# Optimization experiments

Measured on AMD Instinct MI355X. Metric: run time of the kernel, lower is better.

Reference implementation:

```python
import jax, jax.numpy as jnp
import numpy as np

B, S, D = 2, 2048, 2048
HQ, HK, HD = 16, 8, 128          # query heads, kv heads, head_dim
EPS = 1e-6
ROPE_THETA = 10000.0
SCALE = HD ** -0.5


def setup_inputs() -> dict:
    key = jax.random.key(0)
    ks = jax.random.split(key, 6)
    s = lambda fan_in: 1.0 / np.sqrt(fan_in)
    return {
        "hidden_states": jax.random.normal(ks[0], (B, S, D), jnp.float32),
        "positions": jnp.arange(S, dtype=jnp.int32),
        "Wq": jax.random.normal(ks[1], (D, HQ * HD), jnp.float32) * s(D),
        "Wk": jax.random.normal(ks[2], (D, HK * HD), jnp.float32) * s(D),
        "Wv": jax.random.normal(ks[3], (D, HK * HD), jnp.float32) * s(D),
        "Wo": jax.random.normal(ks[4], (HQ * HD, D), jnp.float32) * s(HQ * HD),
        "q_norm_w": jnp.ones((HD,), jnp.float32),
        "k_norm_w": jnp.ones((HD,), jnp.float32),
    }


def _rmsnorm(x, w):
    # RMSNorm over last (head_dim) axis, as in q_norm/k_norm
    var = jnp.mean(jnp.square(x), axis=-1, keepdims=True)
    return x * jax.lax.rsqrt(var + EPS) * w


def _rope(x, positions):
    # x: [B, S, H, HD]; rotate_half-style RoPE (Qwen3 convention)
    half = HD // 2
    inv_freq = 1.0 / (ROPE_THETA ** (jnp.arange(0, half, dtype=jnp.float32) / half))
    angles = positions.astype(jnp.float32)[:, None] * inv_freq[None, :]  # [S, half]
    cos = jnp.cos(angles)[None, :, None, :]  # [1, S, 1, half]
    sin = jnp.sin(angles)[None, :, None, :]
    x1, x2 = x[..., :half], x[..., half:]
    return jnp.concatenate([x1 * cos - x2 * sin, x2 * cos + x1 * sin], axis=-1)


def reference(hidden_states, positions, Wq, Wk, Wv, Wo, q_norm_w, k_norm_w):
    b, s, _ = hidden_states.shape
    q = (hidden_states @ Wq).reshape(b, s, HQ, HD)
    k = (hidden_states @ Wk).reshape(b, s, HK, HD)
    v = (hidden_states @ Wv).reshape(b, s, HK, HD)

    q = _rmsnorm(q, q_norm_w)
    k = _rmsnorm(k, k_norm_w)

    q = _rope(q, positions)
    k = _rope(k, positions)

    # GQA: repeat KV heads to match query heads
    groups = HQ // HK
    k = jnp.repeat(k, groups, axis=2)  # [B, S, HQ, HD]
    v = jnp.repeat(v, groups, axis=2)

    scores = jnp.einsum("bqhd,bkhd->bhqk", q, k) * SCALE  # [B, HQ, S, S]
    causal = jnp.tril(jnp.ones((s, s), dtype=bool))
    scores = jnp.where(causal[None, None], scores, jnp.float32(-jnp.inf))
    attn = jax.nn.softmax(scores, axis=-1)

    out = jnp.einsum("bhqk,bkhd->bqhd", attn, v).reshape(b, s, HQ * HD)
    return out @ Wo
```

## Files before the change

kernel.cpp:

```cpp
#include <hip/hip_runtime.h>
#include <cstdint>
#include <cstddef>

typedef _Float16 half8 __attribute__((ext_vector_type(8)));
typedef _Float16 half4 __attribute__((ext_vector_type(4)));
typedef float f32x4 __attribute__((ext_vector_type(4)));

#define DI __device__ __forceinline__

DI void gld_lds16(void* sp, const void* gp) {
  __builtin_amdgcn_global_load_lds(
      (const __attribute__((address_space(1))) void*)gp,
      (__attribute__((address_space(3))) void*)sp, 16, 0, 0);
}

__global__ __launch_bounds__(256) void prep(const float* __restrict__ hs,
                                            const float* __restrict__ Wq,
                                            const float* __restrict__ Wk,
                                            const float* __restrict__ Wv,
                                            const float* __restrict__ Wo,
                                            _Float16* __restrict__ Xh,
                                            _Float16* __restrict__ Wqkvt,
                                            _Float16* __restrict__ Wot) {
  const int bid = blockIdx.x;
  if (bid >= 12288) {
    const int i = (bid - 12288) * 256 + threadIdx.x;
    const float4* p = (const float4*)hs + (size_t)i * 2;
    const float4 a = p[0], b = p[1];
    half8 h;
    h[0] = (_Float16)a.x; h[1] = (_Float16)a.y; h[2] = (_Float16)a.z; h[3] = (_Float16)a.w;
    h[4] = (_Float16)b.x; h[5] = (_Float16)b.y; h[6] = (_Float16)b.z; h[7] = (_Float16)b.w;
    *(half8*)(Xh + (size_t)i * 8) = h;
    return;
  }
  const float* in;
  _Float16* outp;
  int C, t;
  if (bid < 4096)      { in = Wq; outp = Wqkvt;                        C = 2048; t = bid; }
  else if (bid < 6144) { in = Wk; outp = Wqkvt + (size_t)2048 * 2048;  C = 1024; t = bid - 4096; }
  else if (bid < 8192) { in = Wv; outp = Wqkvt + (size_t)3072 * 2048;  C = 1024; t = bid - 6144; }
  else                 { in = Wo; outp = Wot;                          C = 2048; t = bid - 8192; }
  __shared__ float tl[32][33];
  const int tx = threadIdx.x & 31, ty = threadIdx.x >> 5;
  const int ctiles = C >> 5;
  const int tc = t % ctiles, tr = t / ctiles;
  const int r0 = tr * 32, c0 = tc * 32;
#pragma unroll
  for (int i = 0; i < 4; i++)
    tl[ty + 8 * i][tx] = in[(size_t)(r0 + ty + 8 * i) * C + c0 + tx];
  __syncthreads();
#pragma unroll
  for (int i = 0; i < 4; i++) {
    const int rr = ty + 8 * i;
    outp[(size_t)(c0 + rr) * 2048 + r0 + tx] = (_Float16)tl[tx][rr];
  }
}

template <int BM, bool F16OUT>
__global__ __launch_bounds__(256) void gemm_bt(const _Float16* __restrict__ A,
                                               const _Float16* __restrict__ Bt,
                                               void* __restrict__ Cv,
                                               int M, int N, int K) {
  constexpr int MF = BM / 32;
  constexpr int LA = BM / 64;
  __shared__ _Float16 sA[2][BM * 32];
  __shared__ _Float16 sB[2][128 * 32];
  const int tid = threadIdx.x;
  const int w = tid >> 6, l = tid & 63, lo = l & 15, hi = l >> 4;
  const int gx = gridDim.x, nwg = gx * gridDim.y;
  int bid = blockIdx.y * gx + blockIdx.x;
  bid = (bid & 7) * (nwg >> 3) + (bid >> 3);
  const int bn0 = (bid % gx) * 128, bm0 = (bid / gx) * BM;
  const int wm = w >> 1, wn = w & 1;
  const int srow = l >> 2;
  const int csel = ((l & 3) ^ ((l >> 3) & 3)) * 8;
  const int kswz = (hi ^ ((lo >> 1) & 3)) * 8;

  f32x4 acc[MF][4];
#pragma unroll
  for (int mi = 0; mi < MF; mi++)
#pragma unroll
    for (int ni = 0; ni < 4; ni++)
#pragma unroll
      for (int r = 0; r < 4; r++) acc[mi][ni][r] = 0.0f;

  auto stage = [&](int bi, int kt) {
#pragma unroll
    for (int i = 0; i < LA; ++i) {
      const int j = LA * w + i;
      gld_lds16(&sA[bi][j * 512],
                A + (size_t)(bm0 + j * 16 + srow) * K + (size_t)kt * 32 + csel);
    }
#pragma unroll
    for (int i = 0; i < 2; ++i) {
      const int j = 2 * w + i;
      gld_lds16(&sB[bi][j * 512],
                Bt + (size_t)(bn0 + j * 16 + srow) * K + (size_t)kt * 32 + csel);
    }
  };

  stage(0, 0);
  __syncthreads();
  const int KT = K >> 5;
#pragma unroll 1
  for (int kt = 0; kt < KT; ++kt) {
    const int cur = kt & 1;
    if (kt + 1 < KT) stage(cur ^ 1, kt + 1);
    half8 a[MF], b[4];
#pragma unroll
    for (int mi = 0; mi < MF; mi++)
      a[mi] = *(const half8*)&sA[cur][(wm * (BM / 2) + mi * 16 + lo) * 32 + kswz];
#pragma unroll
    for (int ni = 0; ni < 4; ni++)
      b[ni] = *(const half8*)&sB[cur][(wn * 64 + ni * 16 + lo) * 32 + kswz];
#pragma unroll
    for (int mi = 0; mi < MF; mi++)
#pragma unroll
      for (int ni = 0; ni < 4; ni++)
        acc[mi][ni] = __builtin_amdgcn_mfma_f32_16x16x32_f16(a[mi], b[ni], acc[mi][ni], 0, 0, 0);
    __syncthreads();
  }

#pragma unroll
  for (int mi = 0; mi < MF; mi++)
#pragma unroll
    for (int ni = 0; ni < 4; ni++)
#pragma unroll
      for (int r = 0; r < 4; r++) {
        const size_t idx = (size_t)(bm0 + wm * (BM / 2) + mi * 16 + hi * 4 + r) * N +
                           (bn0 + wn * 64 + ni * 16 + lo);
        if constexpr (F16OUT) ((_Float16*)Cv)[idx] = (_Float16)acc[mi][ni][r];
        else                  ((float*)Cv)[idx] = acc[mi][ni][r];
      }
}

__global__ __launch_bounds__(256) void post(const float* __restrict__ QKV,
                                            const int* __restrict__ pos,
                                            const float* __restrict__ qw,
                                            const float* __restrict__ kw,
                                            _Float16* __restrict__ Qb,
                                            _Float16* __restrict__ Kb,
                                            _Float16* __restrict__ Vt) {
  if (blockIdx.x >= 24576) {
    __shared__ float tt[32][33];
    const int g = blockIdx.x - 24576;
    const int tx = threadIdx.x & 31, ty = threadIdx.x >> 5;
    const int dt = g & 3;
    const int st = (g >> 2) & 63;
    const int bh = g >> 8;
    const float* src = QKV + (size_t)((bh >> 3) * 2048 + st * 32) * 4096 +
                       3072 + (bh & 7) * 128 + dt * 32;
#pragma unroll
    for (int i = 0; i < 4; i++)
      tt[ty + 8 * i][tx] = src[(size_t)(ty + 8 * i) * 4096 + tx];
    __syncthreads();
    _Float16* dst = Vt + ((size_t)bh * 128 + dt * 32) * 2048 + st * 32;
#pragma unroll
    for (int i = 0; i < 4; i++) {
      const int rr = ty + 8 * i;
      dst[(size_t)rr * 2048 + tx] = (_Float16)tt[tx][rr];
    }
    return;
  }
  const int w = threadIdx.x >> 6, l = threadIdx.x & 63;
  const int wv = blockIdx.x * 4 + w;
  const int t = wv / 24, hh = wv - t * 24;
  const int b = t >> 11, s = t & 2047;
  const bool isq = hh < 16;
  const int col = isq ? hh * 128 : 2048 + (hh - 16) * 128;
  const float* x = QKV + (size_t)t * 4096 + col;
  const float x1 = x[l], x2 = x[l + 64];
  float ss = x1 * x1 + x2 * x2;
  ss += __shfl_xor(ss, 32); ss += __shfl_xor(ss, 16); ss += __shfl_xor(ss, 8);
  ss += __shfl_xor(ss, 4);  ss += __shfl_xor(ss, 2);  ss += __shfl_xor(ss, 1);
  const float rn = rsqrtf(ss * 0.0078125f + 1e-6f);
  const float* wt = isq ? qw : kw;
  const float n1 = x1 * rn * wt[l], n2 = x2 * rn * wt[l + 64];
  const float ang = (float)pos[s] * exp2f((float)l * -0.2076205059304601f);
  float sa, ca;
  sincosf(ang, &sa, &ca);
  const float qs = isq ? 0.12751731f : 1.0f;
  const float o1 = (n1 * ca - n2 * sa) * qs;
  const float o2 = (n2 * ca + n1 * sa) * qs;
  _Float16* dst = isq ? Qb + (((size_t)b * 16 + hh) * 2048 + s) * 128
                      : Kb + (((size_t)b * 8 + (hh - 16)) * 2048 + s) * 128;
  dst[l] = (_Float16)o1;
  dst[l + 64] = (_Float16)o2;
}

__global__ __launch_bounds__(256) void attn_fwd(const _Float16* __restrict__ Q,
                                                const _Float16* __restrict__ K,
                                                const _Float16* __restrict__ Vt,
                                                _Float16* __restrict__ AO) {
  __shared__ _Float16 sK[2][64 * 128];
  __shared__ _Float16 sV[2][128 * 64];
  __shared__ _Float16 P[4][16 * 80];
  const int tid = threadIdx.x, w = tid >> 6, l = tid & 63, lo = l & 15, hi = l >> 4;
  const int qt = 31 - (blockIdx.x >> 5);
  const int hq = blockIdx.x & 15;
  const int b = (blockIdx.x >> 4) & 1;
  const int hk = hq >> 1, q0 = qt * 64;
  const _Float16* Qh = Q + ((size_t)(b * 16 + hq) * 2048) * 128;
  const _Float16* Kh = K + ((size_t)(b * 8 + hk) * 2048) * 128;
  const _Float16* Vh = Vt + ((size_t)(b * 8 + hk) * 128) * 2048;
  const int qw0 = q0 + w * 16;

  auto stageK = [&](int bi, int kv0) {
#pragma unroll
    for (int i = 0; i < 4; ++i) {
      const int inst = w * 4 + i;
      const int r = inst * 4 + (l >> 4);
      const int cb = ((l & 15) * 16) ^ ((r & 7) << 4);
      gld_lds16(&sK[bi][inst * 512],
                (const char*)Kh + (size_t)(kv0 + r) * 256 + cb);
    }
  };
  auto stageV = [&](int bi, int kv0) {
#pragma unroll
    for (int i = 0; i < 4; ++i) {
      const int inst = w * 4 + i;
      const int r = inst * 8 + (l >> 3);
      const int cb = ((l & 7) * 16) ^ ((r & 7) << 4);
      gld_lds16(&sV[bi][inst * 512],
                (const char*)Vh + (size_t)r * 4096 + (size_t)kv0 * 2 + cb);
    }
  };

  half8 aq[4];
#pragma unroll
  for (int kc = 0; kc < 4; kc++)
    aq[kc] = *(const half8*)(Qh + (size_t)(qw0 + lo) * 128 + kc * 32 + hi * 8);

  f32x4 o[8];
#pragma unroll
  for (int dn = 0; dn < 8; dn++)
#pragma unroll
    for (int r = 0; r < 4; r++) o[dn][r] = 0.0f;
  float mrow = -1e30f, lrow = 0.0f;

  const int nt = qt + 1;
  stageK(0, 0);
  stageV(0, 0);
  __syncthreads();
#pragma unroll 1
  for (int kt = 0; kt < nt; ++kt) {
    const int kv0 = kt * 64;
    const int cur = kt & 1;
    if (kt + 1 < nt) {
      stageK(cur ^ 1, kv0 + 64);
      stageV(cur ^ 1, kv0 + 64);
    }
    const char* kb = (const char*)sK[cur];
    const char* vb = (const char*)sV[cur];
    f32x4 s[4];
#pragma unroll
    for (int ns = 0; ns < 4; ns++) {
#pragma unroll
      for (int r = 0; r < 4; r++) s[ns][r] = 0.0f;
      const int krow = ns * 16 + lo;
#pragma unroll
      for (int kc = 0; kc < 4; kc++) {
        half8 bk = *(const half8*)(kb + krow * 256 +
                                   ((kc * 64 + hi * 16) ^ ((krow & 7) << 4)));
        s[ns] = __builtin_amdgcn_mfma_f32_16x16x32_f16(bk, aq[kc], s[ns], 0, 0, 0);
      }
    }
    if (kt == nt - 1) {
#pragma unroll
      for (int ns = 0; ns < 4; ns++) {
        const int kv = kv0 + ns * 16 + hi * 4;
#pragma unroll
        for (int r = 0; r < 4; r++)
          if (kv + r > qw0 + lo) s[ns][r] = -1e30f;
      }
    }
    float tmax = s[0][0];
#pragma unroll
    for (int ns = 0; ns < 4; ns++)
#pragma unroll
      for (int r = 0; r < 4; r++) tmax = fmaxf(tmax, s[ns][r]);
    tmax = fmaxf(tmax, __shfl_xor(tmax, 16));
    tmax = fmaxf(tmax, __shfl_xor(tmax, 32));
    if (!__all(tmax <= mrow + 8.0f)) {
      const float mn = fmaxf(mrow, tmax);
      const float corr = exp2f(mrow - mn);
      mrow = mn;
      lrow *= corr;
      float c4[4];
#pragma unroll
      for (int r = 0; r < 4; r++) c4[r] = __shfl(corr, hi * 4 + r, 16);
#pragma unroll
      for (int dn = 0; dn < 8; dn++)
#pragma unroll
        for (int r = 0; r < 4; r++) o[dn][r] *= c4[r];
    }
    float psum = 0.0f;
#pragma unroll
    for (int ns = 0; ns < 4; ns++) {
      half4 pk;
#pragma unroll
      for (int r = 0; r < 4; r++) {
        const float p = exp2f(s[ns][r] - mrow);
        psum += p;
        pk[r] = (_Float16)p;
      }
      *(half4*)&P[w][lo * 80 + ns * 16 + hi * 4] = pk;
    }
    psum += __shfl_xor(psum, 16);
    psum += __shfl_xor(psum, 32);
    lrow += psum;
    asm volatile("s_waitcnt lgkmcnt(0)" ::: "memory");
    half8 ap0 = *(const half8*)&P[w][lo * 80 + hi * 8];
    half8 ap1 = *(const half8*)&P[w][lo * 80 + 32 + hi * 8];
#pragma unroll
    for (int dn = 0; dn < 8; dn++) {
      const int vrow = dn * 16 + lo;
      half8 bv0 = *(const half8*)(vb + vrow * 128 + ((hi * 16) ^ ((vrow & 7) << 4)));
      half8 bv1 = *(const half8*)(vb + vrow * 128 + ((64 + hi * 16) ^ ((vrow & 7) << 4)));
      o[dn] = __builtin_amdgcn_mfma_f32_16x16x32_f16(ap0, bv0, o[dn], 0, 0, 0);
      o[dn] = __builtin_amdgcn_mfma_f32_16x16x32_f16(ap1, bv1, o[dn], 0, 0, 0);
    }
    __syncthreads();
  }

  const float inv = 1.0f / lrow;
  float i4[4];
#pragma unroll
  for (int r = 0; r < 4; r++) i4[r] = __shfl(inv, hi * 4 + r, 16);
  const size_t tok = (size_t)b * 2048 + qw0;
#pragma unroll
  for (int dn = 0; dn < 8; dn++)
#pragma unroll
    for (int r = 0; r < 4; r++)
      AO[(tok + hi * 4 + r) * 2048 + hq * 128 + dn * 16 + lo] = (_Float16)(o[dn][r] * i4[r]);
}

extern "C" void kernel_launch(void* const* d_in, const int* in_sizes, int n_in,
                              void* d_out, int out_size, void* d_ws, size_t ws_size,
                              hipStream_t stream) {
  (void)in_sizes; (void)n_in; (void)out_size; (void)ws_size;
  const float* hs  = (const float*)d_in[0];
  const int*   pos = (const int*)d_in[1];
  const float* Wq  = (const float*)d_in[2];
  const float* Wk  = (const float*)d_in[3];
  const float* Wv  = (const float*)d_in[4];
  const float* Wo  = (const float*)d_in[5];
  const float* qnw = (const float*)d_in[6];
  const float* knw = (const float*)d_in[7];
  float* out = (float*)d_out;

  char* ws = (char*)d_ws;
  size_t off = 0;
  auto take = [&](size_t bytes) -> void* {
    void* p = ws + off;
    off += (bytes + 255) & ~(size_t)255;
    return p;
  };
  _Float16* Xh    = (_Float16*)take((size_t)4096 * 2048 * 2);
  _Float16* Wqkvt = (_Float16*)take((size_t)4096 * 2048 * 2);
  _Float16* Wot   = (_Float16*)take((size_t)2048 * 2048 * 2);
  float*    QKV   = (float*)take((size_t)4096 * 4096 * 4);
  _Float16* Qb    = (_Float16*)take((size_t)2 * 16 * 2048 * 128 * 2);
  _Float16* Kb    = (_Float16*)take((size_t)2 * 8 * 2048 * 128 * 2);
  _Float16* Vt    = (_Float16*)take((size_t)2 * 8 * 128 * 2048 * 2);
  _Float16* AO    = (_Float16*)take((size_t)4096 * 2048 * 2);

  prep<<<16384, 256, 0, stream>>>(hs, Wq, Wk, Wv, Wo, Xh, Wqkvt, Wot);
  gemm_bt<128, false><<<dim3(32, 32), 256, 0, stream>>>(Xh, Wqkvt, QKV, 4096, 4096, 2048);
  post<<<28672, 256, 0, stream>>>(QKV, pos, qnw, knw, Qb, Kb, Vt);
  attn_fwd<<<1024, 256, 0, stream>>>(Qb, Kb, Vt, AO);
  gemm_bt<64, false><<<dim3(16, 64), 256, 0, stream>>>(AO, Wot, out, 4096, 2048, 2048);
}
```

Before: 250.5 us.

## Replace QKV projection GEMM with 256x256-tile pipelined 512-thread kernel

Adds a new gemm256 kernel for the fused QKV projection. It uses 256x256 output tiles, 8 waves, a triple-buffered A and double-buffered B LDS pipeline with direct global-to-LDS loads, and a swizzled layout. Loads for future k-tiles are interleaved across four MFMA phases with raw barriers, explicit vmcnt waits and setprio to hide memory latency. The goal is more data reuse per tile and better overlap of loads with compute. In exchange it needs a large LDS footprint (160KB per block) and launches only 256 blocks.

Result: faster. 236.1 us (-5.7%).

```diff
diff --git a/kernel.cpp b/kernel.cpp
--- a/kernel.cpp
+++ b/kernel.cpp
@@ -12,6 +12,15 @@
   __builtin_amdgcn_global_load_lds(
       (const __attribute__((address_space(1))) void*)gp,
       (__attribute__((address_space(3))) void*)sp, 16, 0, 0);
+}
+
+template <int N>
+DI void vmwait() { asm volatile("s_waitcnt vmcnt(%0)" :: "n"(N) : "memory"); }
+
+DI void barrier_raw() {
+  asm volatile("" ::: "memory");
+  __builtin_amdgcn_s_barrier();
+  asm volatile("" ::: "memory");
 }
 
 __global__ __launch_bounds__(256) void prep(const float* __restrict__ hs,
@@ -54,6 +63,109 @@
     const int rr = ty + 8 * i;
     outp[(size_t)(c0 + rr) * 2048 + r0 + tx] = (_Float16)tl[tx][rr];
   }
+}
+
+#define QPHASE(Q, STAGE, VMW)                                                  \
+  {                                                                            \
+    half8 afr[2][2];                                                           \
+    _Pragma("unroll") for (int j = 0; j < 2; j++)                              \
+      _Pragma("unroll") for (int ks = 0; ks < 2; ks++) {                       \
+        const int arow = wm * 128 + ((Q) * 2 + j) * 16 + lo;                   \
+        afr[j][ks] =                                                           \
+            *(const half8*)&sA[sa][arow * 64 + (((ks * 4 + hi) ^ lo7) << 3)];  \
+      }                                                                        \
+    STAGE;                                                                     \
+    VMW;                                                                       \
+    barrier_raw();                                                             \
+    asm volatile("s_waitcnt lgkmcnt(0)" ::: "memory");                         \
+    __builtin_amdgcn_sched_barrier(0);                                         \
+    __builtin_amdgcn_s_setprio(1);                                             \
+    _Pragma("unroll") for (int j = 0; j < 2; j++)                              \
+      _Pragma("unroll") for (int nf = 0; nf < 4; nf++)                         \
+        _Pragma("unroll") for (int ks = 0; ks < 2; ks++)                       \
+          acc[(Q) * 2 + j][nf] = __builtin_amdgcn_mfma_f32_16x16x32_f16(       \
+              afr[j][ks], bfr[nf][ks], acc[(Q) * 2 + j][nf], 0, 0, 0);         \
+    __builtin_amdgcn_s_setprio(0);                                             \
+    barrier_raw();                                                             \
+  }
+
+__global__ __launch_bounds__(512, 2) void gemm256(const _Float16* __restrict__ A,
+                                                  const _Float16* __restrict__ Bt,
+                                                  float* __restrict__ C,
+                                                  int M, int N, int K) {
+  __shared__ _Float16 sA[3][16384];
+  __shared__ _Float16 sB[2][16384];
+  const int tid = threadIdx.x, w = tid >> 6, l = tid & 63, lo = l & 15, hi = l >> 4;
+  const int lo7 = lo & 7;
+  const int wm = w >> 2, wn = w & 3;
+  const int nbn = N >> 8;
+  const int nwg = gridDim.x;
+  int bid = blockIdx.x;
+  bid = (bid & 7) * (nwg >> 3) + (bid >> 3);
+  const int bm0 = (bid / nbn) << 8, bn0 = (bid % nbn) << 8;
+  const int cswz = ((tid & 7) ^ ((tid >> 3) & 7)) << 3;
+  const int NT = K >> 6;
+
+  auto stageA = [&](int kt, int slot, int i0) {
+#pragma unroll
+    for (int ii = 0; ii < 2; ++ii) {
+      const int i = i0 + ii;
+      gld_lds16(&sA[slot][i * 4096 + (w << 9)],
+                A + (size_t)(bm0 + i * 64 + (tid >> 3)) * K + kt * 64 + cswz);
+    }
+  };
+  auto stageB = [&](int kt, int slot, int i0) {
+#pragma unroll
+    for (int ii = 0; ii < 2; ++ii) {
+      const int i = i0 + ii;
+      gld_lds16(&sB[slot][i * 4096 + (w << 9)],
+                Bt + (size_t)(bn0 + i * 64 + (tid >> 3)) * K + kt * 64 + cswz);
+    }
+  };
+
+  f32x4 acc[8][4];
+#pragma unroll
+  for (int mf = 0; mf < 8; mf++)
+#pragma unroll
+    for (int nf = 0; nf < 4; nf++)
+#pragma unroll
+      for (int r = 0; r < 4; r++) acc[mf][nf][r] = 0.0f;
+
+  stageA(0, 0, 0); stageA(0, 0, 2);
+  stageA(1, 1, 0); stageA(1, 1, 2);
+  stageB(0, 0, 0); stageB(0, 0, 2);
+  vmwait<0>();
+  barrier_raw();
+
+  int sa = 0, sa2 = 2;
+#pragma unroll 1
+  for (int t = 0; t < NT; ++t) {
+    const int sb = t & 1, sb1 = sb ^ 1;
+    half8 bfr[4][2];
+#pragma unroll
+    for (int nf = 0; nf < 4; nf++)
+#pragma unroll
+      for (int ks = 0; ks < 2; ks++) {
+        const int brow = wn * 64 + nf * 16 + lo;
+        bfr[nf][ks] = *(const half8*)&sB[sb][brow * 64 + (((ks * 4 + hi) ^ lo7) << 3)];
+      }
+    QPHASE(0, if (t + 1 < NT) stageB(t + 1, sb1, 0), )
+    QPHASE(1, if (t + 1 < NT) stageB(t + 1, sb1, 2), )
+    QPHASE(2, if (t + 2 < NT) stageA(t + 2, sa2, 0), )
+    QPHASE(3, if (t + 2 < NT) stageA(t + 2, sa2, 2),
+           if (t + 2 < NT) { vmwait<4>(); } else { vmwait<0>(); })
+    sa = (sa == 2) ? 0 : sa + 1;
+    sa2 = (sa2 == 2) ? 0 : sa2 + 1;
+  }
+
+#pragma unroll
+  for (int mf = 0; mf < 8; mf++)
+#pragma unroll
+    for (int nf = 0; nf < 4; nf++)
+#pragma unroll
+      for (int r = 0; r < 4; r++)
+        C[(size_t)(bm0 + wm * 128 + mf * 16 + hi * 4 + r) * N +
+          (bn0 + wn * 64 + nf * 16 + lo)] = acc[mf][nf][r];
 }
 
 template <int BM, bool F16OUT>
@@ -366,7 +478,7 @@
   _Float16* AO    = (_Float16*)take((size_t)4096 * 2048 * 2);
 
   prep<<<16384, 256, 0, stream>>>(hs, Wq, Wk, Wv, Wo, Xh, Wqkvt, Wot);
-  gemm_bt<128, false><<<dim3(32, 32), 256, 0, stream>>>(Xh, Wqkvt, QKV, 4096, 4096, 2048);
+  gemm256<<<256, 512, 0, stream>>>(Xh, Wqkvt, QKV, 4096, 4096, 2048);
   post<<<28672, 256, 0, stream>>>(QKV, pos, qnw, knw, Qb, Kb, Vt);
   attn_fwd<<<1024, 256, 0, stream>>>(Qb, Kb, Vt, AO);
   gemm_bt<64, false><<<dim3(16, 64), 256, 0, stream>>>(AO, Wot, out, 4096, 2048, 2048);
```
